# Kernel tuning notes

Hardware: AMD Instinct MI355X
Metric: run time of the kernel (lower is better)

Reference implementation:

```python
import jax, jax.numpy as jnp
import numpy as np
from jax import lax

EPS = 1e-5
NPOINT = 2048
RADIUS = 0.2
K = 32


def fps(xyz, npoint):
    # Farthest point sampling, deterministic start at index 0. xyz: (B,N,3)
    B, N, _ = xyz.shape
    big = jnp.asarray(1e10, xyz.dtype)
    init_idx = jnp.zeros((B,), jnp.int32)

    def body(carry, _):
        mind, last = carry
        p = jnp.take_along_axis(xyz, last[:, None, None], axis=1)  # (B,1,3)
        d = jnp.sum((xyz - p) ** 2, axis=-1)                        # (B,N)
        mind = jnp.minimum(mind, d)
        nxt = jnp.argmax(mind, axis=-1).astype(jnp.int32)
        return (mind, nxt), nxt

    (_, _), rest = lax.scan(body, (jnp.full((B, N), big, xyz.dtype), init_idx), None, length=npoint - 1)
    return jnp.concatenate([init_idx[None], rest], axis=0).T  # (B, npoint)


def ball_query(xyz, new_xyz, radius, k):
    # Euclidean cdist via |a|^2 + |b|^2 - 2ab to avoid a (B,S,N,3) intermediate.
    a2 = jnp.sum(new_xyz ** 2, -1)[:, :, None]            # (B,S,1)
    b2 = jnp.sum(xyz ** 2, -1)[:, None, :]                # (B,1,N)
    ab = jnp.einsum('bsc,bnc->bsn', new_xyz, xyz)         # (B,S,N)
    dists = jnp.sqrt(jnp.maximum(a2 + b2 - 2.0 * ab, 0.0))
    order = jnp.argsort(dists, axis=-1)[..., :k]          # (B,S,k)
    gd = jnp.take_along_axis(dists, order, axis=-1)
    return jnp.where(gd < radius, order, -1)


def group_points(points, idx):
    # points: (B,N,C), idx: (B,S,k) with -1 sentinel -> clamp to 0 (matches torch code)
    B, S, k = idx.shape
    C = points.shape[-1]
    idxc = jnp.where(idx < 0, 0, idx).reshape(B, S * k)
    g = jnp.take_along_axis(points, idxc[:, :, None], axis=1)
    return g.reshape(B, S, k, C)


def reference(xyz, features, W0, b0, g0, be0, m0, v0, W1, b1, g1, be1, m1, v1, W2, b2, g2, be2, m2, v2):
    B, N, _ = xyz.shape
    sidx = fps(xyz, NPOINT)                                    # (B,S)
    new_xyz = jnp.take_along_axis(xyz, sidx[:, :, None], axis=1)  # (B,S,3)
    idx = ball_query(xyz, new_xyz, RADIUS, K)                  # (B,S,k)
    grouped_xyz = group_points(xyz, idx) - new_xyz[:, :, None, :]  # (B,S,k,3)
    grouped_feat = group_points(features, idx)                 # (B,S,k,C)
    x = jnp.concatenate([grouped_xyz, grouped_feat], axis=-1)  # (B,S,k,3+C)
    for W, b, g, be, m, v in ((W0, b0, g0, be0, m0, v0), (W1, b1, g1, be1, m1, v1), (W2, b2, g2, be2, m2, v2)):
        x = jnp.einsum('bskc,oc->bsko', x, W) + b              # 1x1 Conv2d
        x = (x - m) * (g / jnp.sqrt(v + EPS)) + be             # BatchNorm2d (inference)
        x = jax.nn.relu(x)
    new_features = jnp.max(x, axis=2)                          # max over k neighbors -> (B,S,128)
    return new_xyz, new_features


def setup_inputs() -> dict:
    key = jax.random.key(0)
    ks = jax.random.split(key, 24)
    B, N, C = 8, 8192, 64
    inp = {
        'xyz': jax.random.uniform(ks[0], (B, N, 3), jnp.float32),
        'features': jax.random.normal(ks[1], (B, N, C), jnp.float32),
    }
    dims = [(64, 67), (64, 64), (128, 64)]
    for i, (o, c) in enumerate(dims):
        base = 2 + i * 6
        inp[f'W{i}'] = jax.random.normal(ks[base], (o, c), jnp.float32) * 0.1
        inp[f'b{i}'] = jax.random.normal(ks[base + 1], (o,), jnp.float32) * 0.1
        inp[f'g{i}'] = jax.random.uniform(ks[base + 2], (o,), jnp.float32, 0.5, 1.5)
        inp[f'be{i}'] = jax.random.normal(ks[base + 3], (o,), jnp.float32) * 0.1
        inp[f'm{i}'] = jax.random.normal(ks[base + 4], (o,), jnp.float32) * 0.1
        inp[f'v{i}'] = jax.random.uniform(ks[base + 5], (o,), jnp.float32, 0.5, 1.5)
    return inp
```

## Files before the change

### kernel.cpp

```cpp
#include <hip/hip_runtime.h>

typedef __attribute__((ext_vector_type(8))) short short8;
typedef __attribute__((ext_vector_type(4))) float f32x4;
typedef __attribute__((ext_vector_type(2))) float f32x2;

#define NPTS 8192
#define NCTR 2048
#define CANDCAP 1536

__device__ __forceinline__ short f2bf(float f) {
  unsigned u = __float_as_uint(f);
  u += 0x7fffu + ((u >> 16) & 1u);
  return (short)(u >> 16);
}

template <int CTRL, int RM>
__device__ __forceinline__ unsigned long long dppmax64(unsigned long long k) {
  int lo = (int)(unsigned)k;
  int hi = (int)(unsigned)(k >> 32);
  int plo = __builtin_amdgcn_update_dpp(lo, lo, CTRL, RM, 0xf, false);
  int phi = __builtin_amdgcn_update_dpp(hi, hi, CTRL, RM, 0xf, false);
  unsigned long long o = ((unsigned long long)(unsigned)phi << 32) | (unsigned)(unsigned)plo;
  return (o > k) ? o : k;
}
template <int CTRL, int RM>
__device__ __forceinline__ unsigned long long dppmin64(unsigned long long k) {
  int lo = (int)(unsigned)k;
  int hi = (int)(unsigned)(k >> 32);
  int plo = __builtin_amdgcn_update_dpp(lo, lo, CTRL, RM, 0xf, false);
  int phi = __builtin_amdgcn_update_dpp(hi, hi, CTRL, RM, 0xf, false);
  unsigned long long o = ((unsigned long long)(unsigned)phi << 32) | (unsigned)(unsigned)plo;
  return (o < k) ? o : k;
}
__device__ __forceinline__ unsigned long long wave_max64(unsigned long long k) {
  k = dppmax64<0xB1, 0xF>(k);
  k = dppmax64<0x4E, 0xF>(k);
  k = dppmax64<0x141, 0xF>(k);
  k = dppmax64<0x140, 0xF>(k);
  k = dppmax64<0x142, 0xA>(k);
  k = dppmax64<0x143, 0xC>(k);
  return k;
}
__device__ __forceinline__ unsigned long long wave_min64(unsigned long long k) {
  k = dppmin64<0xB1, 0xF>(k);
  k = dppmin64<0x4E, 0xF>(k);
  k = dppmin64<0x141, 0xF>(k);
  k = dppmin64<0x140, 0xF>(k);
  k = dppmin64<0x142, 0xA>(k);
  k = dppmin64<0x143, 0xC>(k);
  return k;
}
__device__ __forceinline__ unsigned long long wave_bcast63(unsigned long long k) {
  unsigned lo = (unsigned)__builtin_amdgcn_readlane((int)(unsigned)k, 63);
  unsigned hi = (unsigned)__builtin_amdgcn_readlane((int)(unsigned)(k >> 32), 63);
  return ((unsigned long long)hi << 32) | lo;
}
__device__ __forceinline__ unsigned long long umin64(unsigned long long a, unsigned long long b) {
  return a < b ? a : b;
}

__global__ __launch_bounds__(256) void fps_kernel(const float* __restrict__ xyz,
                                                  float* __restrict__ newxyz) {
#pragma clang fp contract(off)
  __shared__ float xs[NPTS], ys[NPTS], zs[NPTS];
  __shared__ unsigned long long wkeys[2][4];
  const int b = blockIdx.x;
  const int t = threadIdx.x;
  const float* xb = xyz + (size_t)b * NPTS * 3;
  for (int i = t; i < NPTS * 3; i += 256) {
    float v = xb[i];
    int p = i / 3;
    int c = i - p * 3;
    if (c == 0) xs[p] = v; else if (c == 1) ys[p] = v; else zs[p] = v;
  }
  __syncthreads();
  f32x2 X2[16], Y2[16], Z2[16];
  float MD[32];
#pragma unroll
  for (int j = 0; j < 16; ++j) {
    int p0 = t + ((2 * j) << 8);
    int p1 = t + ((2 * j + 1) << 8);
    X2[j] = (f32x2){xs[p0], xs[p1]};
    Y2[j] = (f32x2){ys[p0], ys[p1]};
    Z2[j] = (f32x2){zs[p0], zs[p1]};
    MD[2 * j] = 1e10f;
    MD[2 * j + 1] = 1e10f;
  }
  float px = xs[0], py = ys[0], pz = zs[0];
  if (t == 0) {
    size_t ob = (size_t)b * NCTR * 3;
    newxyz[ob] = px; newxyz[ob + 1] = py; newxyz[ob + 2] = pz;
  }
  const int lane = t & 63;
  const int wid = t >> 6;
  for (int it = 1; it < NCTR; ++it) {
    const f32x2 px2 = (f32x2){px, px};
    const f32x2 py2 = (f32x2){py, py};
    const f32x2 pz2 = (f32x2){pz, pz};
#pragma unroll
    for (int j = 0; j < 16; ++j) {
      f32x2 dx = X2[j] - px2;
      f32x2 dy = Y2[j] - py2;
      f32x2 dz = Z2[j] - pz2;
      f32x2 q0 = dx * dx;
      f32x2 q1 = dy * dy;
      f32x2 q2 = dz * dz;
      f32x2 d = (q0 + q1) + q2;
      MD[2 * j] = fminf(MD[2 * j], d.x);
      MD[2 * j + 1] = fminf(MD[2 * j + 1], d.y);
    }
    float m[16];
#pragma unroll
    for (int j = 0; j < 16; ++j) m[j] = fmaxf(MD[2 * j], MD[2 * j + 1]);
#pragma unroll
    for (int j = 0; j < 8; ++j) m[j] = fmaxf(m[2 * j], m[2 * j + 1]);
#pragma unroll
    for (int j = 0; j < 4; ++j) m[j] = fmaxf(m[2 * j], m[2 * j + 1]);
    float bv = fmaxf(fmaxf(m[0], m[1]), fmaxf(m[2], m[3]));
    int bp = 0;
#pragma unroll
    for (int j = 31; j >= 0; --j)
      if (MD[j] == bv) bp = t + (j << 8);
    unsigned long long key =
        ((unsigned long long)__float_as_uint(bv) << 32) | (unsigned long long)(8191 - bp);
    key = wave_bcast63(wave_max64(key));
    if (lane == 0) wkeys[it & 1][wid] = key;
    __syncthreads();
    unsigned long long k0 = wkeys[it & 1][0];
    unsigned long long k1 = wkeys[it & 1][1];
    unsigned long long k2 = wkeys[it & 1][2];
    unsigned long long k3 = wkeys[it & 1][3];
    unsigned long long ka = k0 > k1 ? k0 : k1;
    unsigned long long kb = k2 > k3 ? k2 : k3;
    unsigned long long kg = ka > kb ? ka : kb;
    const int idxw = 8191 - (int)(kg & 0xffffffffull);
    px = xs[idxw]; py = ys[idxw]; pz = zs[idxw];
    if (t == 0) {
      size_t ob = ((size_t)b * NCTR + it) * 3;
      newxyz[ob] = px; newxyz[ob + 1] = py; newxyz[ob + 2] = pz;
    }
  }
}

__global__ __launch_bounds__(256) void ballq_kernel(const float* __restrict__ xyz,
                                                    const float* __restrict__ newxyz,
                                                    int* __restrict__ nbr) {
#pragma clang fp contract(off)
  __shared__ float xs[NPTS], ys[NPTS], zs[NPTS];
  __shared__ unsigned long long cand[4][CANDCAP];
  __shared__ int outidx[4][32];
  const int blk = blockIdx.x;
  const int b = blk >> 6;
  const int grp = blk & 63;
  const float* xb = xyz + (size_t)b * NPTS * 3;
  for (int i = threadIdx.x; i < NPTS * 3; i += 256) {
    float v = xb[i];
    int p = i / 3;
    int c = i - p * 3;
    if (c == 0) xs[p] = v; else if (c == 1) ys[p] = v; else zs[p] = v;
  }
  __syncthreads();
  const int wid = threadIdx.x >> 6;
  const int lane = threadIdx.x & 63;
  for (int ci = 0; ci < 8; ++ci) {
    const int s = grp * 32 + wid * 8 + ci;
    const float* c3 = newxyz + ((size_t)b * NCTR + s) * 3;
    float cx = c3[0], cy = c3[1], cz = c3[2];
    float a2 = (cx * cx + cy * cy) + cz * cz;
    int base = 0;
    for (int p0 = 0; p0 < NPTS; p0 += 64) {
      int p = p0 + lane;
      float bx = xs[p], by = ys[p], bz = zs[p];
      float b2 = (bx * bx + by * by) + bz * bz;
      float ab = fmaf(cz, bz, fmaf(cy, by, cx * bx));
      float s2 = (a2 + b2) - 2.0f * ab;
      s2 = fmaxf(s2, 0.0f);
      float dist = sqrtf(s2);
      bool in = dist < 0.2f;
      unsigned long long mask = __ballot(in);
      if (in) {
        int pos = base + (int)__popcll(mask & ((1ull << lane) - 1ull));
        if (pos < CANDCAP)
          cand[wid][pos] = ((unsigned long long)__float_as_uint(dist) << 32) | (unsigned)p;
      }
      base += (int)__popcll(mask);
    }
    int m = base < CANDCAP ? base : CANDCAP;
    if (m <= 512) {
      unsigned long long r0 = ~0ull, r1 = ~0ull, r2 = ~0ull, r3 = ~0ull;
      unsigned long long r4 = ~0ull, r5 = ~0ull, r6 = ~0ull, r7 = ~0ull;
      if (lane < m) r0 = cand[wid][lane];
      if (lane + 64 < m) r1 = cand[wid][lane + 64];
      if (lane + 128 < m) r2 = cand[wid][lane + 128];
      if (lane + 192 < m) r3 = cand[wid][lane + 192];
      if (lane + 256 < m) r4 = cand[wid][lane + 256];
      if (lane + 320 < m) r5 = cand[wid][lane + 320];
      if (lane + 384 < m) r6 = cand[wid][lane + 384];
      if (lane + 448 < m) r7 = cand[wid][lane + 448];
      const int nsel = m < 32 ? m : 32;
      for (int tsel = 0; tsel < nsel; ++tsel) {
        unsigned long long ka = umin64(umin64(r0, r1), umin64(r2, r3));
        unsigned long long kb = umin64(umin64(r4, r5), umin64(r6, r7));
        unsigned long long kmin = umin64(ka, kb);
        unsigned long long r = wave_bcast63(wave_min64(kmin));
        r0 = (r0 == r) ? ~0ull : r0;
        r1 = (r1 == r) ? ~0ull : r1;
        r2 = (r2 == r) ? ~0ull : r2;
        r3 = (r3 == r) ? ~0ull : r3;
        r4 = (r4 == r) ? ~0ull : r4;
        r5 = (r5 == r) ? ~0ull : r5;
        r6 = (r6 == r) ? ~0ull : r6;
        r7 = (r7 == r) ? ~0ull : r7;
        if (lane == 0) outidx[wid][tsel] = (int)(r & 0xffffffffull);
      }
      if (lane == 0)
        for (int tsel = nsel; tsel < 32; ++tsel) outidx[wid][tsel] = 0;
    } else {
      for (int tsel = 0; tsel < 32; ++tsel) {
        if (tsel < m) {
          unsigned long long kmin = ~0ull;
          int kslot = -1;
          for (int p = lane; p < m; p += 64) {
            unsigned long long k = cand[wid][p];
            if (k < kmin) { kmin = k; kslot = p; }
          }
          unsigned long long r = wave_bcast63(wave_min64(kmin));
          if (kmin == r && kslot >= 0) cand[wid][kslot] = ~0ull;
          if (lane == 0) outidx[wid][tsel] = (int)(r & 0xffffffffull);
        } else {
          if (lane == 0) outidx[wid][tsel] = 0;
        }
      }
    }
    if (lane < 32) nbr[(((size_t)b * NCTR + s) << 5) + lane] = outidx[wid][lane];
  }
}

__global__ __launch_bounds__(256) void pack_kernel(const float* __restrict__ feat,
                                                   short* __restrict__ featb) {
  const size_t i = (size_t)blockIdx.x * 256 + threadIdx.x;
  const f32x4* src = (const f32x4*)(feat + i * 8);
  f32x4 u = src[0];
  f32x4 v = src[1];
  short8 pk;
  pk[0] = f2bf(u[0]); pk[1] = f2bf(u[1]); pk[2] = f2bf(u[2]); pk[3] = f2bf(u[3]);
  pk[4] = f2bf(v[0]); pk[5] = f2bf(v[1]); pk[6] = f2bf(v[2]); pk[7] = f2bf(v[3]);
  *(short8*)(featb + i * 8) = pk;
}

__global__ __launch_bounds__(256) void prep_kernel(
    const float* __restrict__ W0, const float* __restrict__ b0, const float* __restrict__ g0,
    const float* __restrict__ be0, const float* __restrict__ m0, const float* __restrict__ v0,
    const float* __restrict__ W1, const float* __restrict__ b1, const float* __restrict__ g1,
    const float* __restrict__ be1, const float* __restrict__ m1, const float* __restrict__ v1,
    const float* __restrict__ W2, const float* __restrict__ b2, const float* __restrict__ g2,
    const float* __restrict__ be2, const float* __restrict__ m2, const float* __restrict__ v2,
    short* __restrict__ wfrag, float* __restrict__ tvec) {
  const int tid = threadIdx.x;
  if (tid < 64) {
    float sc = g0[tid] / sqrtf(v0[tid] + 1e-5f);
    tvec[tid] = (b0[tid] - m0[tid]) * sc + be0[tid];
  } else if (tid < 128) {
    int o = tid - 64;
    float sc = g1[o] / sqrtf(v1[o] + 1e-5f);
    tvec[tid] = (b1[o] - m1[o]) * sc + be1[o];
  } else {
    int o = tid - 128;
    float sc = g2[o] / sqrtf(v2[o] + 1e-5f);
    tvec[tid] = (b2[o] - m2[o]) * sc + be2[o];
  }
  for (int idx = tid; idx < 18432; idx += 256) {
    const float *W, *g, *v;
    int rem, NT, L;
    if (idx < 6144)       { L = 0; rem = idx;         W = W0; g = g0; v = v0; NT = 4; }
    else if (idx < 10240) { L = 1; rem = idx - 6144;  W = W1; g = g1; v = v1; NT = 4; }
    else                  { L = 2; rem = idx - 10240; W = W2; g = g2; v = v2; NT = 8; }
    int f = rem >> 9;
    int lane = (rem >> 3) & 63;
    int e = rem & 7;
    int kc = f / NT, ct = f - kc * NT;
    int o = ct * 16 + (lane & 15);
    int k = kc * 32 + ((lane >> 4) << 3) + e;
    float val = 0.0f;
    if (L == 0) {
      if (k < 64) val = W[o * 67 + (k + 3)];
      else if (k < 67) val = W[o * 67 + (k - 64)];
    } else {
      if (k < 64) val = W[o * 64 + k];
    }
    float sc = g[o] / sqrtf(v[o] + 1e-5f);
    wfrag[idx] = f2bf(val * sc);
  }
}

template <bool PACKED>
__global__ __launch_bounds__(256) void mlp_kernel(
    const float* __restrict__ xyz, const float* __restrict__ feat,
    const short* __restrict__ featb,
    const float* __restrict__ newxyz, const int* __restrict__ nbr,
    const short* __restrict__ wfrag, const float* __restrict__ tvec,
    float* __restrict__ outf) {
  __shared__ short Xl[128 * 128];
  __shared__ short Yl[128 * 64];
  const int bid = blockIdx.x;
  const int b = bid >> 9;
  const int g = bid & 511;
  const int w = threadIdx.x >> 6;
  const int lane = threadIdx.x & 63;
  const int s = g * 4 + w;
  {
    const int r = lane & 31;
    const int h = lane >> 5;
    const int row = w * 32 + r;
    const int n = nbr[(((size_t)b * NCTR + s) << 5) + r];
    if (PACKED) {
      const short8* fb8 = (const short8*)(featb + (((size_t)b * NPTS + n) << 6));
#pragma unroll
      for (int c4 = 0; c4 < 4; ++c4) {
        short8 pk = fb8[h * 4 + c4];
        const int chunk = h * 4 + c4;
        *(short8*)&Xl[row * 128 + ((chunk ^ (r & 7)) << 3)] = pk;
      }
    } else {
      const f32x4* fr4 = (const f32x4*)(feat + (((size_t)b * NPTS + n) << 6));
#pragma unroll
      for (int c4 = 0; c4 < 4; ++c4) {
        f32x4 u = fr4[h * 8 + c4 * 2];
        f32x4 v2 = fr4[h * 8 + c4 * 2 + 1];
        short8 pk;
        pk[0] = f2bf(u[0]); pk[1] = f2bf(u[1]); pk[2] = f2bf(u[2]); pk[3] = f2bf(u[3]);
        pk[4] = f2bf(v2[0]); pk[5] = f2bf(v2[1]); pk[6] = f2bf(v2[2]); pk[7] = f2bf(v2[3]);
        const int chunk = h * 4 + c4;
        *(short8*)&Xl[row * 128 + ((chunk ^ (r & 7)) << 3)] = pk;
      }
    }
    if (h == 0) {
      const float* pn = xyz + ((size_t)b * NPTS + n) * 3;
      const float* cc = newxyz + ((size_t)b * NCTR + s) * 3;
      short8 pk = {0, 0, 0, 0, 0, 0, 0, 0};
      pk[0] = f2bf(pn[0] - cc[0]);
      pk[1] = f2bf(pn[1] - cc[1]);
      pk[2] = f2bf(pn[2] - cc[2]);
      *(short8*)&Xl[row * 128 + ((8 ^ (r & 7)) << 3)] = pk;
      short8 z = {0, 0, 0, 0, 0, 0, 0, 0};
      *(short8*)&Xl[row * 128 + ((9 ^ (r & 7)) << 3)] = z;
      *(short8*)&Xl[row * 128 + ((10 ^ (r & 7)) << 3)] = z;
      *(short8*)&Xl[row * 128 + ((11 ^ (r & 7)) << 3)] = z;
    }
  }
  const int ar = lane & 15;
  const int ah = lane >> 4;
  const short8* wf8 = (const short8*)wfrag;
  f32x4 acc[2][4];
  const f32x4 zf = {0.f, 0.f, 0.f, 0.f};
#pragma unroll
  for (int mt = 0; mt < 2; ++mt)
#pragma unroll
    for (int ct = 0; ct < 4; ++ct) acc[mt][ct] = zf;
#pragma unroll
  for (int kc = 0; kc < 3; ++kc) {
    const int csw = (((kc << 2) + ah) ^ (ar & 7)) << 3;
    short8 a0 = *(const short8*)&Xl[(w * 32 + ar) * 128 + csw];
    short8 a1 = *(const short8*)&Xl[(w * 32 + 16 + ar) * 128 + csw];
#pragma unroll
    for (int ct = 0; ct < 4; ++ct) {
      short8 bf = wf8[(kc * 4 + ct) * 64 + lane];
      acc[0][ct] = __builtin_amdgcn_mfma_f32_16x16x32_bf16(a0, bf, acc[0][ct], 0, 0, 0);
      acc[1][ct] = __builtin_amdgcn_mfma_f32_16x16x32_bf16(a1, bf, acc[1][ct], 0, 0, 0);
    }
  }
#pragma unroll
  for (int mt = 0; mt < 2; ++mt)
#pragma unroll
    for (int ct = 0; ct < 4; ++ct) {
      const float tc = tvec[ct * 16 + ar];
      const int col = ct * 16 + ar;
#pragma unroll
      for (int q = 0; q < 4; ++q) {
        const int orow = w * 32 + mt * 16 + ah * 4 + q;
        float y = fmaxf(acc[mt][ct][q] + tc, 0.f);
        Yl[orow * 64 + (((col >> 3) ^ (orow & 7)) << 3) + (col & 7)] = f2bf(y);
      }
    }
#pragma unroll
  for (int mt = 0; mt < 2; ++mt)
#pragma unroll
    for (int ct = 0; ct < 4; ++ct) acc[mt][ct] = zf;
#pragma unroll
  for (int kc = 0; kc < 2; ++kc) {
    const int csw = (((kc << 2) + ah) ^ (ar & 7)) << 3;
    short8 a0 = *(const short8*)&Yl[(w * 32 + ar) * 64 + csw];
    short8 a1 = *(const short8*)&Yl[(w * 32 + 16 + ar) * 64 + csw];
#pragma unroll
    for (int ct = 0; ct < 4; ++ct) {
      short8 bf = wf8[768 + (kc * 4 + ct) * 64 + lane];
      acc[0][ct] = __builtin_amdgcn_mfma_f32_16x16x32_bf16(a0, bf, acc[0][ct], 0, 0, 0);
      acc[1][ct] = __builtin_amdgcn_mfma_f32_16x16x32_bf16(a1, bf, acc[1][ct], 0, 0, 0);
    }
  }
#pragma unroll
  for (int mt = 0; mt < 2; ++mt)
#pragma unroll
    for (int ct = 0; ct < 4; ++ct) {
      const float tc = tvec[64 + ct * 16 + ar];
      const int col = ct * 16 + ar;
#pragma unroll
      for (int q = 0; q < 4; ++q) {
        const int orow = w * 32 + mt * 16 + ah * 4 + q;
        float y = fmaxf(acc[mt][ct][q] + tc, 0.f);
        Yl[orow * 64 + (((col >> 3) ^ (orow & 7)) << 3) + (col & 7)] = f2bf(y);
      }
    }
#pragma unroll
  for (int nh = 0; nh < 2; ++nh) {
#pragma unroll
    for (int mt = 0; mt < 2; ++mt)
#pragma unroll
      for (int ct = 0; ct < 4; ++ct) acc[mt][ct] = zf;
#pragma unroll
    for (int kc = 0; kc < 2; ++kc) {
      const int csw = (((kc << 2) + ah) ^ (ar & 7)) << 3;
      short8 a0 = *(const short8*)&Yl[(w * 32 + ar) * 64 + csw];
      short8 a1 = *(const short8*)&Yl[(w * 32 + 16 + ar) * 64 + csw];
#pragma unroll
      for (int ct = 0; ct < 4; ++ct) {
        short8 bf = wf8[1280 + (kc * 8 + nh * 4 + ct) * 64 + lane];
        acc[0][ct] = __builtin_amdgcn_mfma_f32_16x16x32_bf16(a0, bf, acc[0][ct], 0, 0, 0);
        acc[1][ct] = __builtin_amdgcn_mfma_f32_16x16x32_bf16(a1, bf, acc[1][ct], 0, 0, 0);
      }
    }
    float vv[4];
#pragma unroll
    for (int ct = 0; ct < 4; ++ct) {
      float pmax = fmaxf(
          fmaxf(fmaxf(acc[0][ct][0], acc[0][ct][1]), fmaxf(acc[0][ct][2], acc[0][ct][3])),
          fmaxf(fmaxf(acc[1][ct][0], acc[1][ct][1]), fmaxf(acc[1][ct][2], acc[1][ct][3])));
      pmax = fmaxf(pmax, __shfl_xor(pmax, 16));
      pmax = fmaxf(pmax, __shfl_xor(pmax, 32));
      vv[ct] = fmaxf(pmax + tvec[128 + nh * 64 + ct * 16 + ar], 0.f);
    }
    float vout = (ah == 0) ? vv[0] : (ah == 1) ? vv[1] : (ah == 2) ? vv[2] : vv[3];
    outf[(((size_t)b * NCTR + s) << 7) + nh * 64 + (ah << 4) + ar] = vout;
  }
}

extern "C" void kernel_launch(void* const* d_in, const int* in_sizes, int n_in,
                              void* d_out, int out_size, void* d_ws, size_t ws_size,
                              hipStream_t stream) {
  const float* xyz = (const float*)d_in[0];
  const float* feat = (const float*)d_in[1];
  const float* P[18];
  for (int i = 0; i < 18; ++i) P[i] = (const float*)d_in[2 + i];

  char* ws = (char*)d_ws;
  int* nbr = (int*)ws;
  short* wfrag = (short*)(ws + 2097152);
  float* tvec = (float*)(ws + 2134016);
  short* featb = (short*)(ws + 2135040);
  const bool packed = ws_size >= (2135040ull + 8388608ull);

  float* newxyz = (float*)d_out;
  float* outf = (float*)d_out + 49152;

  if (packed) pack_kernel<<<dim3(2048), dim3(256), 0, stream>>>(feat, featb);
  prep_kernel<<<dim3(1), dim3(256), 0, stream>>>(
      P[0], P[1], P[2], P[3], P[4], P[5],
      P[6], P[7], P[8], P[9], P[10], P[11],
      P[12], P[13], P[14], P[15], P[16], P[17],
      wfrag, tvec);
  fps_kernel<<<dim3(8), dim3(256), 0, stream>>>(xyz, newxyz);
  ballq_kernel<<<dim3(512), dim3(256), 0, stream>>>(xyz, newxyz, nbr);
  if (packed)
    mlp_kernel<true><<<dim3(4096), dim3(256), 0, stream>>>(xyz, feat, featb, newxyz, nbr, wfrag, tvec, outf);
  else
    mlp_kernel<false><<<dim3(4096), dim3(256), 0, stream>>>(xyz, feat, featb, newxyz, nbr, wfrag, tvec, outf);
}
```

Before: 2.458 ms.

## Fuse FPS, ball query and MLP into one producer-consumer persistent kernel

Merges the three kernels into a single launch. Eight producer blocks run farthest point sampling and publish progress counters with release stores every 16 centers. 128 consumer blocks spin on those counters and run the ball query plus the fused MLP for each center as soon as it is available. This overlaps the serial FPS with the downstream work and drops the neighbour-index round trip through global memory. The cost is that consumers occupy CUs while spinning, and correctness depends on producers and consumers all being resident at the same time.

```diff
diff --git a/kernel.cpp b/kernel.cpp
--- a/kernel.cpp
+++ b/kernel.cpp
@@ -7,6 +7,8 @@
 #define NPTS 8192
 #define NCTR 2048
 #define CANDCAP 1536
+#define NPROD 8
+#define NCONS 128
 
 __device__ __forceinline__ short f2bf(float f) {
   unsigned u = __float_as_uint(f);
@@ -59,180 +61,320 @@
   return a < b ? a : b;
 }
 
-__global__ __launch_bounds__(256) void fps_kernel(const float* __restrict__ xyz,
-                                                  float* __restrict__ newxyz) {
-#pragma clang fp contract(off)
-  __shared__ float xs[NPTS], ys[NPTS], zs[NPTS];
-  __shared__ unsigned long long wkeys[2][4];
-  const int b = blockIdx.x;
-  const int t = threadIdx.x;
-  const float* xb = xyz + (size_t)b * NPTS * 3;
-  for (int i = t; i < NPTS * 3; i += 256) {
-    float v = xb[i];
-    int p = i / 3;
-    int c = i - p * 3;
-    if (c == 0) xs[p] = v; else if (c == 1) ys[p] = v; else zs[p] = v;
-  }
-  __syncthreads();
-  f32x2 X2[16], Y2[16], Z2[16];
-  float MD[32];
-#pragma unroll
-  for (int j = 0; j < 16; ++j) {
-    int p0 = t + ((2 * j) << 8);
-    int p1 = t + ((2 * j + 1) << 8);
-    X2[j] = (f32x2){xs[p0], xs[p1]};
-    Y2[j] = (f32x2){ys[p0], ys[p1]};
-    Z2[j] = (f32x2){zs[p0], zs[p1]};
-    MD[2 * j] = 1e10f;
-    MD[2 * j + 1] = 1e10f;
-  }
-  float px = xs[0], py = ys[0], pz = zs[0];
-  if (t == 0) {
-    size_t ob = (size_t)b * NCTR * 3;
-    newxyz[ob] = px; newxyz[ob + 1] = py; newxyz[ob + 2] = pz;
-  }
-  const int lane = t & 63;
-  const int wid = t >> 6;
-  for (int it = 1; it < NCTR; ++it) {
-    const f32x2 px2 = (f32x2){px, px};
-    const f32x2 py2 = (f32x2){py, py};
-    const f32x2 pz2 = (f32x2){pz, pz};
-#pragma unroll
-    for (int j = 0; j < 16; ++j) {
-      f32x2 dx = X2[j] - px2;
-      f32x2 dy = Y2[j] - py2;
-      f32x2 dz = Z2[j] - pz2;
-      f32x2 q0 = dx * dx;
-      f32x2 q1 = dy * dy;
-      f32x2 q2 = dz * dz;
-      f32x2 d = (q0 + q1) + q2;
-      MD[2 * j] = fminf(MD[2 * j], d.x);
-      MD[2 * j + 1] = fminf(MD[2 * j + 1], d.y);
-    }
-    float m[16];
-#pragma unroll
-    for (int j = 0; j < 16; ++j) m[j] = fmaxf(MD[2 * j], MD[2 * j + 1]);
-#pragma unroll
-    for (int j = 0; j < 8; ++j) m[j] = fmaxf(m[2 * j], m[2 * j + 1]);
-#pragma unroll
-    for (int j = 0; j < 4; ++j) m[j] = fmaxf(m[2 * j], m[2 * j + 1]);
-    float bv = fmaxf(fmaxf(m[0], m[1]), fmaxf(m[2], m[3]));
-    int bp = 0;
-#pragma unroll
-    for (int j = 31; j >= 0; --j)
-      if (MD[j] == bv) bp = t + (j << 8);
-    unsigned long long key =
-        ((unsigned long long)__float_as_uint(bv) << 32) | (unsigned long long)(8191 - bp);
-    key = wave_bcast63(wave_max64(key));
-    if (lane == 0) wkeys[it & 1][wid] = key;
-    __syncthreads();
-    unsigned long long k0 = wkeys[it & 1][0];
-    unsigned long long k1 = wkeys[it & 1][1];
-    unsigned long long k2 = wkeys[it & 1][2];
-    unsigned long long k3 = wkeys[it & 1][3];
-    unsigned long long ka = k0 > k1 ? k0 : k1;
-    unsigned long long kb = k2 > k3 ? k2 : k3;
-    unsigned long long kg = ka > kb ? ka : kb;
-    const int idxw = 8191 - (int)(kg & 0xffffffffull);
-    px = xs[idxw]; py = ys[idxw]; pz = zs[idxw];
-    if (t == 0) {
-      size_t ob = ((size_t)b * NCTR + it) * 3;
-      newxyz[ob] = px; newxyz[ob + 1] = py; newxyz[ob + 2] = pz;
-    }
-  }
-}
-
-__global__ __launch_bounds__(256) void ballq_kernel(const float* __restrict__ xyz,
-                                                    const float* __restrict__ newxyz,
-                                                    int* __restrict__ nbr) {
+template <bool PACKED>
+__global__ __launch_bounds__(256) void mega_kernel(
+    const float* __restrict__ xyz, const float* __restrict__ feat,
+    const short* __restrict__ featb, const short* __restrict__ wfrag,
+    const float* __restrict__ tvecg, unsigned* __restrict__ prog,
+    float* __restrict__ newxyz, float* __restrict__ outf) {
 #pragma clang fp contract(off)
   __shared__ float xs[NPTS], ys[NPTS], zs[NPTS];
   __shared__ unsigned long long cand[4][CANDCAP];
   __shared__ int outidx[4][32];
-  const int blk = blockIdx.x;
-  const int b = blk >> 6;
-  const int grp = blk & 63;
-  const float* xb = xyz + (size_t)b * NPTS * 3;
-  for (int i = threadIdx.x; i < NPTS * 3; i += 256) {
-    float v = xb[i];
-    int p = i / 3;
-    int c = i - p * 3;
-    if (c == 0) xs[p] = v; else if (c == 1) ys[p] = v; else zs[p] = v;
-  }
-  __syncthreads();
-  const int wid = threadIdx.x >> 6;
-  const int lane = threadIdx.x & 63;
-  for (int ci = 0; ci < 8; ++ci) {
-    const int s = grp * 32 + wid * 8 + ci;
-    const float* c3 = newxyz + ((size_t)b * NCTR + s) * 3;
-    float cx = c3[0], cy = c3[1], cz = c3[2];
-    float a2 = (cx * cx + cy * cy) + cz * cz;
-    int base = 0;
-    for (int p0 = 0; p0 < NPTS; p0 += 64) {
-      int p = p0 + lane;
-      float bx = xs[p], by = ys[p], bz = zs[p];
-      float b2 = (bx * bx + by * by) + bz * bz;
-      float ab = fmaf(cz, bz, fmaf(cy, by, cx * bx));
-      float s2 = (a2 + b2) - 2.0f * ab;
-      s2 = fmaxf(s2, 0.0f);
-      float dist = sqrtf(s2);
-      bool in = dist < 0.2f;
-      unsigned long long mask = __ballot(in);
-      if (in) {
-        int pos = base + (int)__popcll(mask & ((1ull << lane) - 1ull));
-        if (pos < CANDCAP)
-          cand[wid][pos] = ((unsigned long long)__float_as_uint(dist) << 32) | (unsigned)p;
-      }
-      base += (int)__popcll(mask);
-    }
-    int m = base < CANDCAP ? base : CANDCAP;
-    if (m <= 512) {
-      unsigned long long r0 = ~0ull, r1 = ~0ull, r2 = ~0ull, r3 = ~0ull;
-      unsigned long long r4 = ~0ull, r5 = ~0ull, r6 = ~0ull, r7 = ~0ull;
-      if (lane < m) r0 = cand[wid][lane];
-      if (lane + 64 < m) r1 = cand[wid][lane + 64];
-      if (lane + 128 < m) r2 = cand[wid][lane + 128];
-      if (lane + 192 < m) r3 = cand[wid][lane + 192];
-      if (lane + 256 < m) r4 = cand[wid][lane + 256];
-      if (lane + 320 < m) r5 = cand[wid][lane + 320];
-      if (lane + 384 < m) r6 = cand[wid][lane + 384];
-      if (lane + 448 < m) r7 = cand[wid][lane + 448];
-      const int nsel = m < 32 ? m : 32;
-      for (int tsel = 0; tsel < nsel; ++tsel) {
-        unsigned long long ka = umin64(umin64(r0, r1), umin64(r2, r3));
-        unsigned long long kb = umin64(umin64(r4, r5), umin64(r6, r7));
-        unsigned long long kmin = umin64(ka, kb);
-        unsigned long long r = wave_bcast63(wave_min64(kmin));
-        r0 = (r0 == r) ? ~0ull : r0;
-        r1 = (r1 == r) ? ~0ull : r1;
-        r2 = (r2 == r) ? ~0ull : r2;
-        r3 = (r3 == r) ? ~0ull : r3;
-        r4 = (r4 == r) ? ~0ull : r4;
-        r5 = (r5 == r) ? ~0ull : r5;
-        r6 = (r6 == r) ? ~0ull : r6;
-        r7 = (r7 == r) ? ~0ull : r7;
-        if (lane == 0) outidx[wid][tsel] = (int)(r & 0xffffffffull);
-      }
-      if (lane == 0)
-        for (int tsel = nsel; tsel < 32; ++tsel) outidx[wid][tsel] = 0;
-    } else {
-      for (int tsel = 0; tsel < 32; ++tsel) {
-        if (tsel < m) {
-          unsigned long long kmin = ~0ull;
-          int kslot = -1;
-          for (int p = lane; p < m; p += 64) {
-            unsigned long long k = cand[wid][p];
-            if (k < kmin) { kmin = k; kslot = p; }
-          }
-          unsigned long long r = wave_bcast63(wave_min64(kmin));
-          if (kmin == r && kslot >= 0) cand[wid][kslot] = ~0ull;
+  __shared__ unsigned long long wkeys[2][4];
+  const int t = threadIdx.x;
+  const int lane = t & 63;
+  const int wid = t >> 6;
+
+  if (blockIdx.x < NPROD) {
+    const int b = blockIdx.x;
+    const float* xb = xyz + (size_t)b * NPTS * 3;
+    for (int i = t; i < NPTS * 3; i += 256) {
+      float v = xb[i];
+      int p = i / 3;
+      int c = i - p * 3;
+      if (c == 0) xs[p] = v; else if (c == 1) ys[p] = v; else zs[p] = v;
+    }
+    __syncthreads();
+    f32x2 X2[16], Y2[16], Z2[16];
+    float MD[32];
+#pragma unroll
+    for (int j = 0; j < 16; ++j) {
+      int p0 = t + ((2 * j) << 8);
+      int p1 = t + ((2 * j + 1) << 8);
+      X2[j] = (f32x2){xs[p0], xs[p1]};
+      Y2[j] = (f32x2){ys[p0], ys[p1]};
+      Z2[j] = (f32x2){zs[p0], zs[p1]};
+      MD[2 * j] = 1e10f;
+      MD[2 * j + 1] = 1e10f;
+    }
+    float px = xs[0], py = ys[0], pz = zs[0];
+    if (t == 0) {
+      size_t ob = (size_t)b * NCTR * 3;
+      newxyz[ob] = px; newxyz[ob + 1] = py; newxyz[ob + 2] = pz;
+    }
+    for (int it = 1; it < NCTR; ++it) {
+      const f32x2 px2 = (f32x2){px, px};
+      const f32x2 py2 = (f32x2){py, py};
+      const f32x2 pz2 = (f32x2){pz, pz};
+#pragma unroll
+      for (int j = 0; j < 16; ++j) {
+        f32x2 dx = X2[j] - px2;
+        f32x2 dy = Y2[j] - py2;
+        f32x2 dz = Z2[j] - pz2;
+        f32x2 q0 = dx * dx;
+        f32x2 q1 = dy * dy;
+        f32x2 q2 = dz * dz;
+        f32x2 d = (q0 + q1) + q2;
+        MD[2 * j] = fminf(MD[2 * j], d.x);
+        MD[2 * j + 1] = fminf(MD[2 * j + 1], d.y);
+      }
+      float m[16];
+#pragma unroll
+      for (int j = 0; j < 16; ++j) m[j] = fmaxf(MD[2 * j], MD[2 * j + 1]);
+#pragma unroll
+      for (int j = 0; j < 8; ++j) m[j] = fmaxf(m[2 * j], m[2 * j + 1]);
+#pragma unroll
+      for (int j = 0; j < 4; ++j) m[j] = fmaxf(m[2 * j], m[2 * j + 1]);
+      float bv = fmaxf(fmaxf(m[0], m[1]), fmaxf(m[2], m[3]));
+      int bp = 0;
+#pragma unroll
+      for (int j = 31; j >= 0; --j)
+        if (MD[j] == bv) bp = t + (j << 8);
+      unsigned long long key =
+          ((unsigned long long)__float_as_uint(bv) << 32) | (unsigned long long)(8191 - bp);
+      key = wave_bcast63(wave_max64(key));
+      if (lane == 0) wkeys[it & 1][wid] = key;
+      __syncthreads();
+      unsigned long long k0 = wkeys[it & 1][0];
+      unsigned long long k1 = wkeys[it & 1][1];
+      unsigned long long k2 = wkeys[it & 1][2];
+      unsigned long long k3 = wkeys[it & 1][3];
+      unsigned long long ka = k0 > k1 ? k0 : k1;
+      unsigned long long kb = k2 > k3 ? k2 : k3;
+      unsigned long long kg = ka > kb ? ka : kb;
+      const int idxw = 8191 - (int)(kg & 0xffffffffull);
+      px = xs[idxw]; py = ys[idxw]; pz = zs[idxw];
+      if (t == 0) {
+        size_t ob = ((size_t)b * NCTR + it) * 3;
+        newxyz[ob] = px; newxyz[ob + 1] = py; newxyz[ob + 2] = pz;
+        if (((it + 1) & 15) == 0)
+          __hip_atomic_store(&prog[b], (unsigned)(it + 1), __ATOMIC_RELEASE,
+                             __HIP_MEMORY_SCOPE_AGENT);
+      }
+    }
+  } else {
+    const int cons = blockIdx.x - NPROD;
+    const int b = cons & 7;
+    const int cb = cons >> 3;
+    const float* xb = xyz + (size_t)b * NPTS * 3;
+    for (int i = t; i < NPTS * 3; i += 256) {
+      float v = xb[i];
+      int p = i / 3;
+      int c = i - p * 3;
+      if (c == 0) xs[p] = v; else if (c == 1) ys[p] = v; else zs[p] = v;
+    }
+    __syncthreads();
+    const int wv = cb * 4 + wid;
+    const int ar = lane & 15;
+    const int ah = lane >> 4;
+    const short8* wf8 = (const short8*)wfrag;
+    short* Xw = (short*)&cand[wid][0];
+    short* Yw = (short*)&cand[wid][1024];
+    for (int j = 0; j < 32; ++j) {
+      const int s = wv + (j << 6);
+      for (;;) {
+        unsigned pr = __hip_atomic_load(&prog[b], __ATOMIC_ACQUIRE, __HIP_MEMORY_SCOPE_AGENT);
+        if (pr > (unsigned)s) break;
+        __builtin_amdgcn_s_sleep(8);
+      }
+      const float* c3 = newxyz + ((size_t)b * NCTR + s) * 3;
+      float cx = c3[0], cy = c3[1], cz = c3[2];
+      float a2 = (cx * cx + cy * cy) + cz * cz;
+      int base = 0;
+      for (int p0 = 0; p0 < NPTS; p0 += 64) {
+        int p = p0 + lane;
+        float bx = xs[p], by = ys[p], bz = zs[p];
+        float b2 = (bx * bx + by * by) + bz * bz;
+        float ab = fmaf(cz, bz, fmaf(cy, by, cx * bx));
+        float s2 = (a2 + b2) - 2.0f * ab;
+        s2 = fmaxf(s2, 0.0f);
+        float dist = sqrtf(s2);
+        bool in = dist < 0.2f;
+        unsigned long long mask = __ballot(in);
+        if (in) {
+          int pos = base + (int)__popcll(mask & ((1ull << lane) - 1ull));
+          if (pos < CANDCAP)
+            cand[wid][pos] = ((unsigned long long)__float_as_uint(dist) << 32) | (unsigned)p;
+        }
+        base += (int)__popcll(mask);
+      }
+      int m = base < CANDCAP ? base : CANDCAP;
+      if (m <= 512) {
+        unsigned long long r0 = ~0ull, r1 = ~0ull, r2 = ~0ull, r3 = ~0ull;
+        unsigned long long r4 = ~0ull, r5 = ~0ull, r6 = ~0ull, r7 = ~0ull;
+        if (lane < m) r0 = cand[wid][lane];
+        if (lane + 64 < m) r1 = cand[wid][lane + 64];
+        if (lane + 128 < m) r2 = cand[wid][lane + 128];
+        if (lane + 192 < m) r3 = cand[wid][lane + 192];
+        if (lane + 256 < m) r4 = cand[wid][lane + 256];
+        if (lane + 320 < m) r5 = cand[wid][lane + 320];
+        if (lane + 384 < m) r6 = cand[wid][lane + 384];
+        if (lane + 448 < m) r7 = cand[wid][lane + 448];
+        const int nsel = m < 32 ? m : 32;
+        for (int tsel = 0; tsel < nsel; ++tsel) {
+          unsigned long long ka = umin64(umin64(r0, r1), umin64(r2, r3));
+          unsigned long long kb = umin64(umin64(r4, r5), umin64(r6, r7));
+          unsigned long long r = wave_bcast63(wave_min64(umin64(ka, kb)));
+          r0 = (r0 == r) ? ~0ull : r0;
+          r1 = (r1 == r) ? ~0ull : r1;
+          r2 = (r2 == r) ? ~0ull : r2;
+          r3 = (r3 == r) ? ~0ull : r3;
+          r4 = (r4 == r) ? ~0ull : r4;
+          r5 = (r5 == r) ? ~0ull : r5;
+          r6 = (r6 == r) ? ~0ull : r6;
+          r7 = (r7 == r) ? ~0ull : r7;
           if (lane == 0) outidx[wid][tsel] = (int)(r & 0xffffffffull);
+        }
+        if (lane == 0)
+          for (int tsel = nsel; tsel < 32; ++tsel) outidx[wid][tsel] = 0;
+      } else {
+        for (int tsel = 0; tsel < 32; ++tsel) {
+          if (tsel < m) {
+            unsigned long long kmin = ~0ull;
+            int kslot = -1;
+            for (int p = lane; p < m; p += 64) {
+              unsigned long long k = cand[wid][p];
+              if (k < kmin) { kmin = k; kslot = p; }
+            }
+            unsigned long long r = wave_bcast63(wave_min64(kmin));
+            if (kmin == r && kslot >= 0) cand[wid][kslot] = ~0ull;
+            if (lane == 0) outidx[wid][tsel] = (int)(r & 0xffffffffull);
+          } else {
+            if (lane == 0) outidx[wid][tsel] = 0;
+          }
+        }
+      }
+      {
+        const int r = lane & 31;
+        const int h = lane >> 5;
+        const int n = outidx[wid][r];
+        if (PACKED) {
+          const short8* fb8 = (const short8*)(featb + (((size_t)b * NPTS + n) << 6));
+#pragma unroll
+          for (int c4 = 0; c4 < 4; ++c4) {
+            short8 pk = fb8[h * 4 + c4];
+            const int chunk = h * 4 + c4;
+            *(short8*)&Xw[r * 128 + ((chunk ^ (r & 7)) << 3)] = pk;
+          }
         } else {
-          if (lane == 0) outidx[wid][tsel] = 0;
-        }
-      }
-    }
-    if (lane < 32) nbr[(((size_t)b * NCTR + s) << 5) + lane] = outidx[wid][lane];
+          const f32x4* fr4 = (const f32x4*)(feat + (((size_t)b * NPTS + n) << 6));
+#pragma unroll
+          for (int c4 = 0; c4 < 4; ++c4) {
+            f32x4 u = fr4[h * 8 + c4 * 2];
+            f32x4 v2 = fr4[h * 8 + c4 * 2 + 1];
+            short8 pk;
+            pk[0] = f2bf(u[0]); pk[1] = f2bf(u[1]); pk[2] = f2bf(u[2]); pk[3] = f2bf(u[3]);
+            pk[4] = f2bf(v2[0]); pk[5] = f2bf(v2[1]); pk[6] = f2bf(v2[2]); pk[7] = f2bf(v2[3]);
+            const int chunk = h * 4 + c4;
+            *(short8*)&Xw[r * 128 + ((chunk ^ (r & 7)) << 3)] = pk;
+          }
+        }
+        if (h == 0) {
+          const float* pn = xyz + ((size_t)b * NPTS + n) * 3;
+          short8 pk = {0, 0, 0, 0, 0, 0, 0, 0};
+          pk[0] = f2bf(pn[0] - cx);
+          pk[1] = f2bf(pn[1] - cy);
+          pk[2] = f2bf(pn[2] - cz);
+          *(short8*)&Xw[r * 128 + ((8 ^ (r & 7)) << 3)] = pk;
+          short8 z = {0, 0, 0, 0, 0, 0, 0, 0};
+          *(short8*)&Xw[r * 128 + ((9 ^ (r & 7)) << 3)] = z;
+          *(short8*)&Xw[r * 128 + ((10 ^ (r & 7)) << 3)] = z;
+          *(short8*)&Xw[r * 128 + ((11 ^ (r & 7)) << 3)] = z;
+        }
+      }
+      f32x4 acc[2][4];
+      const f32x4 zf = {0.f, 0.f, 0.f, 0.f};
+#pragma unroll
+      for (int mt = 0; mt < 2; ++mt)
+#pragma unroll
+        for (int ct = 0; ct < 4; ++ct) acc[mt][ct] = zf;
+#pragma unroll
+      for (int kc = 0; kc < 3; ++kc) {
+        const int csw = (((kc << 2) + ah) ^ (ar & 7)) << 3;
+        short8 a0 = *(const short8*)&Xw[ar * 128 + csw];
+        short8 a1 = *(const short8*)&Xw[(16 + ar) * 128 + csw];
+#pragma unroll
+        for (int ct = 0; ct < 4; ++ct) {
+          short8 bf = wf8[(kc * 4 + ct) * 64 + lane];
+          acc[0][ct] = __builtin_amdgcn_mfma_f32_16x16x32_bf16(a0, bf, acc[0][ct], 0, 0, 0);
+          acc[1][ct] = __builtin_amdgcn_mfma_f32_16x16x32_bf16(a1, bf, acc[1][ct], 0, 0, 0);
+        }
+      }
+#pragma unroll
+      for (int mt = 0; mt < 2; ++mt)
+#pragma unroll
+        for (int ct = 0; ct < 4; ++ct) {
+          const float tc = tvecg[ct * 16 + ar];
+          const int col = ct * 16 + ar;
+#pragma unroll
+          for (int q = 0; q < 4; ++q) {
+            const int orow = mt * 16 + ah * 4 + q;
+            float y = fmaxf(acc[mt][ct][q] + tc, 0.f);
+            Yw[orow * 64 + (((col >> 3) ^ (orow & 7)) << 3) + (col & 7)] = f2bf(y);
+          }
+        }
+#pragma unroll
+      for (int mt = 0; mt < 2; ++mt)
+#pragma unroll
+        for (int ct = 0; ct < 4; ++ct) acc[mt][ct] = zf;
+#pragma unroll
+      for (int kc = 0; kc < 2; ++kc) {
+        const int csw = (((kc << 2) + ah) ^ (ar & 7)) << 3;
+        short8 a0 = *(const short8*)&Yw[ar * 64 + csw];
+        short8 a1 = *(const short8*)&Yw[(16 + ar) * 64 + csw];
+#pragma unroll
+        for (int ct = 0; ct < 4; ++ct) {
+          short8 bf = wf8[768 + (kc * 4 + ct) * 64 + lane];
+          acc[0][ct] = __builtin_amdgcn_mfma_f32_16x16x32_bf16(a0, bf, acc[0][ct], 0, 0, 0);
+          acc[1][ct] = __builtin_amdgcn_mfma_f32_16x16x32_bf16(a1, bf, acc[1][ct], 0, 0, 0);
+        }
+      }
+#pragma unroll
+      for (int mt = 0; mt < 2; ++mt)
+#pragma unroll
+        for (int ct = 0; ct < 4; ++ct) {
+          const float tc = tvecg[64 + ct * 16 + ar];
+          const int col = ct * 16 + ar;
+#pragma unroll
+          for (int q = 0; q < 4; ++q) {
+            const int orow = mt * 16 + ah * 4 + q;
+            float y = fmaxf(acc[mt][ct][q] + tc, 0.f);
+            Yw[orow * 64 + (((col >> 3) ^ (orow & 7)) << 3) + (col & 7)] = f2bf(y);
+          }
+        }
+#pragma unroll
+      for (int nh = 0; nh < 2; ++nh) {
+#pragma unroll
+        for (int mt = 0; mt < 2; ++mt)
+#pragma unroll
+          for (int ct = 0; ct < 4; ++ct) acc[mt][ct] = zf;
+#pragma unroll
+        for (int kc = 0; kc < 2; ++kc) {
+          const int csw = (((kc << 2) + ah) ^ (ar & 7)) << 3;
+          short8 a0 = *(const short8*)&Yw[ar * 64 + csw];
+          short8 a1 = *(const short8*)&Yw[(16 + ar) * 64 + csw];
+#pragma unroll
+          for (int ct = 0; ct < 4; ++ct) {
+            short8 bf = wf8[1280 + (kc * 8 + nh * 4 + ct) * 64 + lane];
+            acc[0][ct] = __builtin_amdgcn_mfma_f32_16x16x32_bf16(a0, bf, acc[0][ct], 0, 0, 0);
+            acc[1][ct] = __builtin_amdgcn_mfma_f32_16x16x32_bf16(a1, bf, acc[1][ct], 0, 0, 0);
+          }
+        }
+        float vv[4];
+#pragma unroll
+        for (int ct = 0; ct < 4; ++ct) {
+          float pmax = fmaxf(
+              fmaxf(fmaxf(acc[0][ct][0], acc[0][ct][1]), fmaxf(acc[0][ct][2], acc[0][ct][3])),
+              fmaxf(fmaxf(acc[1][ct][0], acc[1][ct][1]), fmaxf(acc[1][ct][2], acc[1][ct][3])));
+          pmax = fmaxf(pmax, __shfl_xor(pmax, 16));
+          pmax = fmaxf(pmax, __shfl_xor(pmax, 32));
+          vv[ct] = fmaxf(pmax + tvecg[128 + nh * 64 + ct * 16 + ar], 0.f);
+        }
+        float vout = (ah == 0) ? vv[0] : (ah == 1) ? vv[1] : (ah == 2) ? vv[2] : vv[3];
+        outf[(((size_t)b * NCTR + s) << 7) + nh * 64 + (ah << 4) + ar] = vout;
+      }
+    }
   }
 }
 
@@ -293,157 +435,6 @@
   }
 }
 
-template <bool PACKED>
-__global__ __launch_bounds__(256) void mlp_kernel(
-    const float* __restrict__ xyz, const float* __restrict__ feat,
-    const short* __restrict__ featb,
-    const float* __restrict__ newxyz, const int* __restrict__ nbr,
-    const short* __restrict__ wfrag, const float* __restrict__ tvec,
-    float* __restrict__ outf) {
-  __shared__ short Xl[128 * 128];
-  __shared__ short Yl[128 * 64];
-  const int bid = blockIdx.x;
-  const int b = bid >> 9;
-  const int g = bid & 511;
-  const int w = threadIdx.x >> 6;
-  const int lane = threadIdx.x & 63;
-  const int s = g * 4 + w;
-  {
-    const int r = lane & 31;
-    const int h = lane >> 5;
-    const int row = w * 32 + r;
-    const int n = nbr[(((size_t)b * NCTR + s) << 5) + r];
-    if (PACKED) {
-      const short8* fb8 = (const short8*)(featb + (((size_t)b * NPTS + n) << 6));
-#pragma unroll
-      for (int c4 = 0; c4 < 4; ++c4) {
-        short8 pk = fb8[h * 4 + c4];
-        const int chunk = h * 4 + c4;
-        *(short8*)&Xl[row * 128 + ((chunk ^ (r & 7)) << 3)] = pk;
-      }
-    } else {
-      const f32x4* fr4 = (const f32x4*)(feat + (((size_t)b * NPTS + n) << 6));
-#pragma unroll
-      for (int c4 = 0; c4 < 4; ++c4) {
-        f32x4 u = fr4[h * 8 + c4 * 2];
-        f32x4 v2 = fr4[h * 8 + c4 * 2 + 1];
-        short8 pk;
-        pk[0] = f2bf(u[0]); pk[1] = f2bf(u[1]); pk[2] = f2bf(u[2]); pk[3] = f2bf(u[3]);
-        pk[4] = f2bf(v2[0]); pk[5] = f2bf(v2[1]); pk[6] = f2bf(v2[2]); pk[7] = f2bf(v2[3]);
-        const int chunk = h * 4 + c4;
-        *(short8*)&Xl[row * 128 + ((chunk ^ (r & 7)) << 3)] = pk;
-      }
-    }
-    if (h == 0) {
-      const float* pn = xyz + ((size_t)b * NPTS + n) * 3;
-      const float* cc = newxyz + ((size_t)b * NCTR + s) * 3;
-      short8 pk = {0, 0, 0, 0, 0, 0, 0, 0};
-      pk[0] = f2bf(pn[0] - cc[0]);
-      pk[1] = f2bf(pn[1] - cc[1]);
-      pk[2] = f2bf(pn[2] - cc[2]);
-      *(short8*)&Xl[row * 128 + ((8 ^ (r & 7)) << 3)] = pk;
-      short8 z = {0, 0, 0, 0, 0, 0, 0, 0};
-      *(short8*)&Xl[row * 128 + ((9 ^ (r & 7)) << 3)] = z;
-      *(short8*)&Xl[row * 128 + ((10 ^ (r & 7)) << 3)] = z;
-      *(short8*)&Xl[row * 128 + ((11 ^ (r & 7)) << 3)] = z;
-    }
-  }
-  const int ar = lane & 15;
-  const int ah = lane >> 4;
-  const short8* wf8 = (const short8*)wfrag;
-  f32x4 acc[2][4];
-  const f32x4 zf = {0.f, 0.f, 0.f, 0.f};
-#pragma unroll
-  for (int mt = 0; mt < 2; ++mt)
-#pragma unroll
-    for (int ct = 0; ct < 4; ++ct) acc[mt][ct] = zf;
-#pragma unroll
-  for (int kc = 0; kc < 3; ++kc) {
-    const int csw = (((kc << 2) + ah) ^ (ar & 7)) << 3;
-    short8 a0 = *(const short8*)&Xl[(w * 32 + ar) * 128 + csw];
-    short8 a1 = *(const short8*)&Xl[(w * 32 + 16 + ar) * 128 + csw];
-#pragma unroll
-    for (int ct = 0; ct < 4; ++ct) {
-      short8 bf = wf8[(kc * 4 + ct) * 64 + lane];
-      acc[0][ct] = __builtin_amdgcn_mfma_f32_16x16x32_bf16(a0, bf, acc[0][ct], 0, 0, 0);
-      acc[1][ct] = __builtin_amdgcn_mfma_f32_16x16x32_bf16(a1, bf, acc[1][ct], 0, 0, 0);
-    }
-  }
-#pragma unroll
-  for (int mt = 0; mt < 2; ++mt)
-#pragma unroll
-    for (int ct = 0; ct < 4; ++ct) {
-      const float tc = tvec[ct * 16 + ar];
-      const int col = ct * 16 + ar;
-#pragma unroll
-      for (int q = 0; q < 4; ++q) {
-        const int orow = w * 32 + mt * 16 + ah * 4 + q;
-        float y = fmaxf(acc[mt][ct][q] + tc, 0.f);
-        Yl[orow * 64 + (((col >> 3) ^ (orow & 7)) << 3) + (col & 7)] = f2bf(y);
-      }
-    }
-#pragma unroll
-  for (int mt = 0; mt < 2; ++mt)
-#pragma unroll
-    for (int ct = 0; ct < 4; ++ct) acc[mt][ct] = zf;
-#pragma unroll
-  for (int kc = 0; kc < 2; ++kc) {
-    const int csw = (((kc << 2) + ah) ^ (ar & 7)) << 3;
-    short8 a0 = *(const short8*)&Yl[(w * 32 + ar) * 64 + csw];
-    short8 a1 = *(const short8*)&Yl[(w * 32 + 16 + ar) * 64 + csw];
-#pragma unroll
-    for (int ct = 0; ct < 4; ++ct) {
-      short8 bf = wf8[768 + (kc * 4 + ct) * 64 + lane];
-      acc[0][ct] = __builtin_amdgcn_mfma_f32_16x16x32_bf16(a0, bf, acc[0][ct], 0, 0, 0);
-      acc[1][ct] = __builtin_amdgcn_mfma_f32_16x16x32_bf16(a1, bf, acc[1][ct], 0, 0, 0);
-    }
-  }
-#pragma unroll
-  for (int mt = 0; mt < 2; ++mt)
-#pragma unroll
-    for (int ct = 0; ct < 4; ++ct) {
-      const float tc = tvec[64 + ct * 16 + ar];
-      const int col = ct * 16 + ar;
-#pragma unroll
-      for (int q = 0; q < 4; ++q) {
-        const int orow = w * 32 + mt * 16 + ah * 4 + q;
-        float y = fmaxf(acc[mt][ct][q] + tc, 0.f);
-        Yl[orow * 64 + (((col >> 3) ^ (orow & 7)) << 3) + (col & 7)] = f2bf(y);
-      }
-    }
-#pragma unroll
-  for (int nh = 0; nh < 2; ++nh) {
-#pragma unroll
-    for (int mt = 0; mt < 2; ++mt)
-#pragma unroll
-      for (int ct = 0; ct < 4; ++ct) acc[mt][ct] = zf;
-#pragma unroll
-    for (int kc = 0; kc < 2; ++kc) {
-      const int csw = (((kc << 2) + ah) ^ (ar & 7)) << 3;
-      short8 a0 = *(const short8*)&Yl[(w * 32 + ar) * 64 + csw];
-      short8 a1 = *(const short8*)&Yl[(w * 32 + 16 + ar) * 64 + csw];
-#pragma unroll
-      for (int ct = 0; ct < 4; ++ct) {
-        short8 bf = wf8[1280 + (kc * 8 + nh * 4 + ct) * 64 + lane];
-        acc[0][ct] = __builtin_amdgcn_mfma_f32_16x16x32_bf16(a0, bf, acc[0][ct], 0, 0, 0);
-        acc[1][ct] = __builtin_amdgcn_mfma_f32_16x16x32_bf16(a1, bf, acc[1][ct], 0, 0, 0);
-      }
-    }
-    float vv[4];
-#pragma unroll
-    for (int ct = 0; ct < 4; ++ct) {
-      float pmax = fmaxf(
-          fmaxf(fmaxf(acc[0][ct][0], acc[0][ct][1]), fmaxf(acc[0][ct][2], acc[0][ct][3])),
-          fmaxf(fmaxf(acc[1][ct][0], acc[1][ct][1]), fmaxf(acc[1][ct][2], acc[1][ct][3])));
-      pmax = fmaxf(pmax, __shfl_xor(pmax, 16));
-      pmax = fmaxf(pmax, __shfl_xor(pmax, 32));
-      vv[ct] = fmaxf(pmax + tvec[128 + nh * 64 + ct * 16 + ar], 0.f);
-    }
-    float vout = (ah == 0) ? vv[0] : (ah == 1) ? vv[1] : (ah == 2) ? vv[2] : vv[3];
-    outf[(((size_t)b * NCTR + s) << 7) + nh * 64 + (ah << 4) + ar] = vout;
-  }
-}
-
 extern "C" void kernel_launch(void* const* d_in, const int* in_sizes, int n_in,
                               void* d_out, int out_size, void* d_ws, size_t ws_size,
                               hipStream_t stream) {
@@ -453,25 +444,26 @@
   for (int i = 0; i < 18; ++i) P[i] = (const float*)d_in[2 + i];
 
   char* ws = (char*)d_ws;
-  int* nbr = (int*)ws;
-  short* wfrag = (short*)(ws + 2097152);
-  float* tvec = (float*)(ws + 2134016);
-  short* featb = (short*)(ws + 2135040);
-  const bool packed = ws_size >= (2135040ull + 8388608ull);
+  unsigned* prog = (unsigned*)ws;
+  short* wfrag = (short*)(ws + 256);
+  float* tvec = (float*)(ws + 37120);
+  short* featb = (short*)(ws + 38400);
+  const bool packed = ws_size >= (38400ull + 8388608ull);
 
   float* newxyz = (float*)d_out;
   float* outf = (float*)d_out + 49152;
 
+  hipMemsetAsync(prog, 0, 64, stream);
   if (packed) pack_kernel<<<dim3(2048), dim3(256), 0, stream>>>(feat, featb);
   prep_kernel<<<dim3(1), dim3(256), 0, stream>>>(
       P[0], P[1], P[2], P[3], P[4], P[5],
       P[6], P[7], P[8], P[9], P[10], P[11],
       P[12], P[13], P[14], P[15], P[16], P[17],
       wfrag, tvec);
-  fps_kernel<<<dim3(8), dim3(256), 0, stream>>>(xyz, newxyz);
-  ballq_kernel<<<dim3(512), dim3(256), 0, stream>>>(xyz, newxyz, nbr);
   if (packed)
-    mlp_kernel<true><<<dim3(4096), dim3(256), 0, stream>>>(xyz, feat, featb, newxyz, nbr, wfrag, tvec, outf);
+    mega_kernel<true><<<dim3(NPROD + NCONS), dim3(256), 0, stream>>>(
+        xyz, feat, featb, wfrag, tvec, prog, newxyz, outf);
   else
-    mlp_kernel<false><<<dim3(4096), dim3(256), 0, stream>>>(xyz, feat, featb, newxyz, nbr, wfrag, tvec, outf);
-}
+    mega_kernel<false><<<dim3(NPROD + NCONS), dim3(256), 0, stream>>>(
+        xyz, feat, featb, wfrag, tvec, prog, newxyz, outf);
+}
```

Result: faster. 2.043 ms (-16.9%).
